# Performance work log

Measured on AMD Instinct MI355X. Metric: run time of the kernel, lower is better.

## Reference

```python
import jax, jax.numpy as jnp
import numpy as np

B, N, D = 4, 1024, 1024
H = 16
HD = D // H
FF = int(D * 2.0)
EPS = 1e-5


def setup_inputs() -> dict:
    key = jax.random.key(0)
    ks = jax.random.split(key, 12)
    s = lambda fan_in: 1.0 / np.sqrt(fan_in)
    return {
        "x": jax.random.normal(ks[0], (B, N, D), dtype=jnp.float32),
        "ln1_g": jnp.ones((D,), jnp.float32),
        "ln1_b": jnp.zeros((D,), jnp.float32),
        "qkv_w": jax.random.normal(ks[1], (D, 3 * D), jnp.float32) * s(D),
        "qkv_b": jnp.zeros((3 * D,), jnp.float32),
        "out_w": jax.random.normal(ks[2], (D, D), jnp.float32) * s(D),
        "out_b": jnp.zeros((D,), jnp.float32),
        "ln2_g": jnp.ones((D,), jnp.float32),
        "ln2_b": jnp.zeros((D,), jnp.float32),
        "w1": jax.random.normal(ks[3], (D, FF), jnp.float32) * s(D),
        "b1": jnp.zeros((FF,), jnp.float32),
        "w2": jax.random.normal(ks[4], (FF, D), jnp.float32) * s(FF),
        "b2": jnp.zeros((D,), jnp.float32),
    }


def _layernorm(x, g, b):
    mu = jnp.mean(x, axis=-1, keepdims=True)
    var = jnp.mean(jnp.square(x - mu), axis=-1, keepdims=True)
    return (x - mu) * jax.lax.rsqrt(var + EPS) * g + b


def _attention(x, qkv_w, qkv_b, out_w, out_b):
    qkv = x @ qkv_w + qkv_b                       # (B,N,3D)
    qkv = qkv.reshape(B, N, 3, H, HD)
    q, k, v = qkv[:, :, 0], qkv[:, :, 1], qkv[:, :, 2]  # (B,N,H,HD)
    scale = 1.0 / np.sqrt(HD)
    attn = jnp.einsum("bnhd,bmhd->bhnm", q, k) * scale
    attn = jax.nn.softmax(attn, axis=-1)
    out = jnp.einsum("bhnm,bmhd->bnhd", attn, v).reshape(B, N, D)
    return out @ out_w + out_b


def reference(x, ln1_g, ln1_b, qkv_w, qkv_b, out_w, out_b, ln2_g, ln2_b, w1, b1, w2, b2):
    x = x + _attention(_layernorm(x, ln1_g, ln1_b), qkv_w, qkv_b, out_w, out_b)
    h = _layernorm(x, ln2_g, ln2_b)
    h = jax.nn.gelu(h @ w1 + b1, approximate=False) @ w2 + b2
    return x + h
```

## Files before the change

kernel.cpp:

```cpp
#include <hip/hip_runtime.h>
#include <hip/hip_bf16.h>
#include <cstdint>
#include <cstddef>

#define Bq 4
#define Nseq 1024
#define Dm 1024
#define Hh 16
#define HDd 64
#define FFd 2048
#define Mrows 4096

typedef __attribute__((ext_vector_type(8))) short bf16x8;
typedef __attribute__((ext_vector_type(4))) float f32x4;
typedef __attribute__((ext_vector_type(16))) float f32x16;

__device__ __forceinline__ void gl_lds16(const void* g, void* l) {
  __builtin_amdgcn_global_load_lds(
      (const __attribute__((address_space(1))) unsigned int*)g,
      (__attribute__((address_space(3))) unsigned int*)l, 16, 0, 0);
}

__device__ __forceinline__ unsigned short f2b(float f) {
  union { __hip_bfloat16 h; unsigned short u; } cv;
  cv.h = __float2bfloat16(f);
  return cv.u;
}

__device__ __forceinline__ unsigned cvt_pk_bf16(float a, float b) {
  unsigned r;
  asm("v_cvt_pk_bf16_f32 %0, %1, %2" : "=v"(r) : "v"(a), "v"(b));
  return r;
}

__device__ __forceinline__ void pl32_swap(unsigned& a, unsigned& b) {
  asm("v_permlane32_swap_b32 %0, %1" : "+v"(a), "+v"(b));
}

__global__ __launch_bounds__(256) void transpose_cast_k(
    const float* __restrict__ src, __hip_bfloat16* __restrict__ dst,
    int K, int Ncols) {
  __shared__ float tile[32][33];
  const int n0 = blockIdx.x * 32, k0 = blockIdx.y * 32;
  const int tx = threadIdx.x & 31, ty = threadIdx.x >> 5;
#pragma unroll
  for (int i = 0; i < 32; i += 8)
    tile[ty + i][tx] = src[(size_t)(k0 + ty + i) * Ncols + n0 + tx];
  __syncthreads();
#pragma unroll
  for (int i = 0; i < 32; i += 8)
    dst[(size_t)(n0 + ty + i) * K + k0 + tx] = __float2bfloat16(tile[tx][ty + i]);
}

__global__ __launch_bounds__(256) void ln_kernel(
    const float* __restrict__ x, const float* __restrict__ gw,
    const float* __restrict__ bw, __hip_bfloat16* __restrict__ out) {
  const int row = blockIdx.x;
  const float4 v = reinterpret_cast<const float4*>(x + (size_t)row * Dm)[threadIdx.x];
  float s1 = v.x + v.y + v.z + v.w;
  float s2 = v.x * v.x + v.y * v.y + v.z * v.z + v.w * v.w;
#pragma unroll
  for (int m = 1; m < 64; m <<= 1) {
    s1 += __shfl_xor(s1, m);
    s2 += __shfl_xor(s2, m);
  }
  __shared__ float a1[4], a2[4];
  const int wv = threadIdx.x >> 6;
  if ((threadIdx.x & 63) == 0) { a1[wv] = s1; a2[wv] = s2; }
  __syncthreads();
  s1 = a1[0] + a1[1] + a1[2] + a1[3];
  s2 = a2[0] + a2[1] + a2[2] + a2[3];
  const float mu = s1 * (1.f / Dm);
  const float rs = rsqrtf(s2 * (1.f / Dm) - mu * mu + 1e-5f);
  const float4 g4 = reinterpret_cast<const float4*>(gw)[threadIdx.x];
  const float4 b4 = reinterpret_cast<const float4*>(bw)[threadIdx.x];
  ushort4 o;
  o.x = f2b((v.x - mu) * rs * g4.x + b4.x);
  o.y = f2b((v.y - mu) * rs * g4.y + b4.y);
  o.z = f2b((v.z - mu) * rs * g4.z + b4.z);
  o.w = f2b((v.w - mu) * rs * g4.w + b4.w);
  reinterpret_cast<ushort4*>(out + (size_t)row * Dm)[threadIdx.x] = o;
}

template <int EPI>
__global__ __launch_bounds__(256, 2) void gemm_bt(
    const __hip_bfloat16* __restrict__ A, const __hip_bfloat16* __restrict__ BT,
    const float* __restrict__ bias, const float* __restrict__ res,
    float* __restrict__ outF, __hip_bfloat16* __restrict__ outB,
    __hip_bfloat16* __restrict__ qb, __hip_bfloat16* __restrict__ kb,
    __hip_bfloat16* __restrict__ vtb, int Ndim, int Kdim) {
  __shared__ alignas(16) __hip_bfloat16 As[128 * 32];
  __shared__ alignas(16) __hip_bfloat16 Bs[128 * 32];
  const int tid = threadIdx.x;
  const int wv = tid >> 6, ln = tid & 63;
  const int wr = wv >> 1, wc = wv & 1;
  const int rowBase = blockIdx.y * 128;
  const int colBase = blockIdx.x * 128;

  f32x4 acc[4][4];
#pragma unroll
  for (int i = 0; i < 4; ++i)
#pragma unroll
    for (int j = 0; j < 4; ++j) acc[i][j] = {0.f, 0.f, 0.f, 0.f};

  const int lr = ln >> 2;
  const int lc = (ln & 3) * 8;
  const int fr = ln & 15, kq = (ln >> 4) * 8;

  for (int k0 = 0; k0 < Kdim; k0 += 32) {
#pragma unroll
    for (int c = 0; c < 2; ++c) {
      const int chunk = c * 4 + wv;
      gl_lds16(A + (size_t)(rowBase + chunk * 16 + lr) * Kdim + k0 + lc,
               (char*)As + chunk * 1024);
      gl_lds16(BT + (size_t)(colBase + chunk * 16 + lr) * Kdim + k0 + lc,
               (char*)Bs + chunk * 1024);
    }
    __syncthreads();
    bf16x8 af[4], bfr[4];
#pragma unroll
    for (int i = 0; i < 4; ++i)
      af[i] = *reinterpret_cast<const bf16x8*>(As + (wr * 64 + i * 16 + fr) * 32 + kq);
#pragma unroll
    for (int j = 0; j < 4; ++j)
      bfr[j] = *reinterpret_cast<const bf16x8*>(Bs + (wc * 64 + j * 16 + fr) * 32 + kq);
#pragma unroll
    for (int i = 0; i < 4; ++i)
#pragma unroll
      for (int j = 0; j < 4; ++j)
        acc[i][j] = __builtin_amdgcn_mfma_f32_16x16x32_bf16(af[i], bfr[j], acc[i][j], 0, 0, 0);
    __syncthreads();
  }

  const int rq = (ln >> 4) * 4;
#pragma unroll
  for (int i = 0; i < 4; ++i) {
#pragma unroll
    for (int j = 0; j < 4; ++j) {
      const int gc = colBase + wc * 64 + j * 16 + fr;
      const float bv = bias[gc];
#pragma unroll
      for (int ii = 0; ii < 4; ++ii) {
        const int gr = rowBase + wr * 64 + i * 16 + rq + ii;
        float v = acc[i][j][ii] + bv;
        if constexpr (EPI == 0) {
          const int which = gc >> 10;
          const int dcol = gc & 1023;
          const int h = dcol >> 6, hd = dcol & 63;
          const int b = gr >> 10, n = gr & 1023;
          const size_t bh = (size_t)(b * Hh + h);
          if (which == 0)
            qb[(bh * Nseq + n) * HDd + hd] = __float2bfloat16(v * 0.125f);
          else if (which == 1)
            kb[(bh * Nseq + n) * HDd + hd] = __float2bfloat16(v);
          else
            vtb[(bh * HDd + hd) * Nseq + n] = __float2bfloat16(v);
        } else if constexpr (EPI == 1) {
          outF[(size_t)gr * Ndim + gc] = v + res[(size_t)gr * Ndim + gc];
        } else {
          outB[(size_t)gr * Ndim + gc] =
              __float2bfloat16(0.5f * v * (1.f + erff(v * 0.70710678118f)));
        }
      }
    }
  }
}

__global__ __launch_bounds__(256, 2) void attn_kernel(
    const __hip_bfloat16* __restrict__ q, const __hip_bfloat16* __restrict__ k,
    const __hip_bfloat16* __restrict__ vt, __hip_bfloat16* __restrict__ attn) {
  __shared__ alignas(16) __hip_bfloat16 Ks[2][64 * 64];
  __shared__ alignas(16) __hip_bfloat16 Vs[2][64 * 64];
  const int tid = threadIdx.x, wv = tid >> 6, ln = tid & 63;
  const int bh = blockIdx.x >> 3, qt = blockIdx.x & 7;
  const int b = bh >> 4, h = bh & 15;
  const int lq = ln & 31;
  const int hl = ln >> 5;

  const __hip_bfloat16* kbase = k + (size_t)bh * Nseq * HDd;
  const __hip_bfloat16* vbase = vt + (size_t)bh * HDd * Nseq;

  const int st_r = ln >> 3;
  const int st_c = (ln & 7) ^ st_r;

  const __hip_bfloat16* qsrc = q + ((size_t)bh * Nseq + qt * 128 + wv * 32 + lq) * HDd;
  bf16x8 qf[4];
#pragma unroll
  for (int s = 0; s < 4; ++s)
    qf[s] = *reinterpret_cast<const bf16x8*>(qsrc + s * 16 + hl * 8);

  float mrun = -1e30f, lrun = 0.f;
  f32x16 ot0 = {}, ot1 = {};

  auto stage = [&](int buf, int kt) {
#pragma unroll
    for (int c = 0; c < 2; ++c) {
      const int chunk = wv * 2 + c;
      gl_lds16(kbase + ((size_t)kt * 64 + chunk * 8 + st_r) * HDd + st_c * 8,
               (char*)&Ks[buf][0] + chunk * 1024);
      gl_lds16(vbase + (size_t)(chunk * 8 + st_r) * Nseq + kt * 64 + st_c * 8,
               (char*)&Vs[buf][0] + chunk * 1024);
    }
  };

  stage(0, 0);
  __syncthreads();
  int cur = 0;

  for (int kt = 0; kt < 16; ++kt) {
    if (kt < 15) stage(cur ^ 1, kt + 1);

    const char* Kp = (const char*)&Ks[cur][0];
    const char* Vp = (const char*)&Vs[cur][0];

    f32x16 st0 = {}, st1 = {};
#pragma unroll
    for (int t = 0; t < 2; ++t) {
      const int row = t * 32 + lq;
#pragma unroll
      for (int s = 0; s < 4; ++s) {
        const bf16x8 kf = *reinterpret_cast<const bf16x8*>(
            Kp + row * 128 + (((s * 2 + hl) ^ (row & 7)) * 16));
        if (t == 0) st0 = __builtin_amdgcn_mfma_f32_32x32x16_bf16(kf, qf[s], st0, 0, 0, 0);
        else        st1 = __builtin_amdgcn_mfma_f32_32x32x16_bf16(kf, qf[s], st1, 0, 0, 0);
      }
    }

    float tmax = st0[0];
#pragma unroll
    for (int r = 1; r < 16; ++r) tmax = fmaxf(tmax, st0[r]);
#pragma unroll
    for (int r = 0; r < 16; ++r) tmax = fmaxf(tmax, st1[r]);
    tmax = fmaxf(tmax, __shfl_xor(tmax, 32));
    const float mn = fmaxf(mrun, tmax);
    const float sc = __expf(mrun - mn);
    mrun = mn;
    float tsum = 0.f;
#pragma unroll
    for (int r = 0; r < 16; ++r) {
      st0[r] = __expf(st0[r] - mn);
      tsum += st0[r];
    }
#pragma unroll
    for (int r = 0; r < 16; ++r) {
      st1[r] = __expf(st1[r] - mn);
      tsum += st1[r];
    }
    tsum += __shfl_xor(tsum, 32);
    lrun = lrun * sc + tsum;
#pragma unroll
    for (int r = 0; r < 16; ++r) { ot0[r] *= sc; ot1[r] *= sc; }

    union PF { unsigned u[4]; bf16x8 v; } pf[4];
#pragma unroll
    for (int t = 0; t < 2; ++t)
#pragma unroll
      for (int g = 0; g < 2; ++g) {
        unsigned w0, w1, w2, w3;
        if (t == 0) {
          w0 = cvt_pk_bf16(st0[g * 8 + 0], st0[g * 8 + 1]);
          w1 = cvt_pk_bf16(st0[g * 8 + 2], st0[g * 8 + 3]);
          w2 = cvt_pk_bf16(st0[g * 8 + 4], st0[g * 8 + 5]);
          w3 = cvt_pk_bf16(st0[g * 8 + 6], st0[g * 8 + 7]);
        } else {
          w0 = cvt_pk_bf16(st1[g * 8 + 0], st1[g * 8 + 1]);
          w1 = cvt_pk_bf16(st1[g * 8 + 2], st1[g * 8 + 3]);
          w2 = cvt_pk_bf16(st1[g * 8 + 4], st1[g * 8 + 5]);
          w3 = cvt_pk_bf16(st1[g * 8 + 6], st1[g * 8 + 7]);
        }
        pl32_swap(w0, w2);
        pl32_swap(w1, w3);
        PF f;
        f.u[0] = w0; f.u[1] = w1; f.u[2] = w2; f.u[3] = w3;
        pf[t * 2 + g] = f;
      }

#pragma unroll
    for (int dt = 0; dt < 2; ++dt) {
      const int row = dt * 32 + lq;
#pragma unroll
      for (int ks = 0; ks < 4; ++ks) {
        const bf16x8 vf = *reinterpret_cast<const bf16x8*>(
            Vp + row * 128 + (((ks * 2 + hl) ^ (row & 7)) * 16));
        if (dt == 0) ot0 = __builtin_amdgcn_mfma_f32_32x32x16_bf16(vf, pf[ks].v, ot0, 0, 0, 0);
        else         ot1 = __builtin_amdgcn_mfma_f32_32x32x16_bf16(vf, pf[ks].v, ot1, 0, 0, 0);
      }
    }

    __syncthreads();
    cur ^= 1;
  }

  const float inv = 1.f / lrun;
  char* swb = (char*)(&Ks[0][0] + wv * 2048);
#pragma unroll
  for (int dt = 0; dt < 2; ++dt)
#pragma unroll
    for (int i = 0; i < 8; ++i) {
      const unsigned w = (dt == 0)
          ? cvt_pk_bf16(ot0[2 * i] * inv, ot0[2 * i + 1] * inv)
          : cvt_pk_bf16(ot1[2 * i] * inv, ot1[2 * i + 1] * inv);
      const int d0 = (2 * i & 2) + 8 * (i >> 1) + 4 * hl + 32 * dt;
      *(unsigned*)(swb + lq * 128 + (((d0 >> 3) ^ (lq & 7)) * 16) + (d0 & 7) * 2) = w;
    }
  const int brow = b * Nseq + qt * 128 + wv * 32;
#pragma unroll
  for (int it = 0; it < 4; ++it) {
    const int qr = it * 8 + (ln >> 3);
    const bf16x8 o = *reinterpret_cast<const bf16x8*>(
        swb + qr * 128 + (((ln & 7) ^ (qr & 7)) * 16));
    *reinterpret_cast<bf16x8*>(attn + (size_t)(brow + qr) * Dm + h * 64 + (ln & 7) * 8) = o;
  }
}

extern "C" void kernel_launch(void* const* d_in, const int* in_sizes, int n_in,
                              void* d_out, int out_size, void* d_ws, size_t ws_size,
                              hipStream_t stream) {
  (void)in_sizes; (void)n_in; (void)out_size; (void)ws_size;
  const float* x     = (const float*)d_in[0];
  const float* ln1_g = (const float*)d_in[1];
  const float* ln1_b = (const float*)d_in[2];
  const float* qkv_w = (const float*)d_in[3];
  const float* qkv_b = (const float*)d_in[4];
  const float* out_w = (const float*)d_in[5];
  const float* out_b = (const float*)d_in[6];
  const float* ln2_g = (const float*)d_in[7];
  const float* ln2_b = (const float*)d_in[8];
  const float* w1    = (const float*)d_in[9];
  const float* b1    = (const float*)d_in[10];
  const float* w2    = (const float*)d_in[11];
  const float* b2    = (const float*)d_in[12];
  float* outp = (float*)d_out;

  char* ws = (char*)d_ws;
  size_t off = 0;
  auto take = [&](size_t bytes) {
    char* p = ws + off;
    off += (bytes + 255) & ~(size_t)255;
    return p;
  };
  __hip_bfloat16* wqkv_t = (__hip_bfloat16*)take((size_t)3 * Dm * Dm * 2);
  __hip_bfloat16* wout_t = (__hip_bfloat16*)take((size_t)Dm * Dm * 2);
  __hip_bfloat16* w1_t   = (__hip_bfloat16*)take((size_t)FFd * Dm * 2);
  __hip_bfloat16* w2_t   = (__hip_bfloat16*)take((size_t)Dm * FFd * 2);
  __hip_bfloat16* xn     = (__hip_bfloat16*)take((size_t)Mrows * Dm * 2);
  __hip_bfloat16* qb     = (__hip_bfloat16*)take((size_t)Mrows * Dm * 2);
  __hip_bfloat16* kb     = (__hip_bfloat16*)take((size_t)Mrows * Dm * 2);
  __hip_bfloat16* vtb    = (__hip_bfloat16*)take((size_t)Mrows * Dm * 2);
  __hip_bfloat16* attn   = (__hip_bfloat16*)take((size_t)Mrows * Dm * 2);
  float*          x1     = (float*)take((size_t)Mrows * Dm * 4);
  __hip_bfloat16* gbuf   = (__hip_bfloat16*)take((size_t)Mrows * FFd * 2);

  const dim3 blk(256);
  transpose_cast_k<<<dim3(3 * Dm / 32, Dm / 32), blk, 0, stream>>>(qkv_w, wqkv_t, Dm, 3 * Dm);
  transpose_cast_k<<<dim3(Dm / 32, Dm / 32), blk, 0, stream>>>(out_w, wout_t, Dm, Dm);
  transpose_cast_k<<<dim3(FFd / 32, Dm / 32), blk, 0, stream>>>(w1, w1_t, Dm, FFd);
  transpose_cast_k<<<dim3(Dm / 32, FFd / 32), blk, 0, stream>>>(w2, w2_t, FFd, Dm);
  ln_kernel<<<dim3(Mrows), blk, 0, stream>>>(x, ln1_g, ln1_b, xn);
  gemm_bt<0><<<dim3(3 * Dm / 128, Mrows / 128), blk, 0, stream>>>(
      xn, wqkv_t, qkv_b, nullptr, nullptr, nullptr, qb, kb, vtb, 3 * Dm, Dm);
  attn_kernel<<<dim3(Bq * Hh * (Nseq / 128)), blk, 0, stream>>>(qb, kb, vtb, attn);
  gemm_bt<1><<<dim3(Dm / 128, Mrows / 128), blk, 0, stream>>>(
      attn, wout_t, out_b, x, x1, nullptr, nullptr, nullptr, nullptr, Dm, Dm);
  ln_kernel<<<dim3(Mrows), blk, 0, stream>>>(x1, ln2_g, ln2_b, xn);
  gemm_bt<2><<<dim3(FFd / 128, Mrows / 128), blk, 0, stream>>>(
      xn, w1_t, b1, nullptr, nullptr, gbuf, nullptr, nullptr, nullptr, FFd, Dm);
  gemm_bt<1><<<dim3(Dm / 128, Mrows / 128), blk, 0, stream>>>(
      gbuf, w2_t, b2, x1, outp, nullptr, nullptr, nullptr, nullptr, Dm, FFd);
}
```

Baseline: 202.4 us.

## Double-buffer GEMM LDS tiles with swizzle and 32x32x16 MFMA

Reworks the bf16 GEMM main loop. It widens the K tile from 32 to 64, double-buffers the A/B tiles in LDS so the next tile's global-to-LDS load overlaps the current MFMAs, and XOR-swizzles the LDS layout to avoid bank conflicts. It also switches from 16x16x32 to 32x32x16 MFMA with a matching epilogue row mapping. LDS use per block grows fourfold, which with launch bounds of 2 blocks per CU may limit occupancy, and the single barrier per iteration relies on async load ordering for correctness.

```diff
diff --git a/kernel.cpp b/kernel.cpp
--- a/kernel.cpp
+++ b/kernel.cpp
@@ -89,60 +89,79 @@
     float* __restrict__ outF, __hip_bfloat16* __restrict__ outB,
     __hip_bfloat16* __restrict__ qb, __hip_bfloat16* __restrict__ kb,
     __hip_bfloat16* __restrict__ vtb, int Ndim, int Kdim) {
-  __shared__ alignas(16) __hip_bfloat16 As[128 * 32];
-  __shared__ alignas(16) __hip_bfloat16 Bs[128 * 32];
+  __shared__ alignas(16) __hip_bfloat16 As[2][128 * 64];
+  __shared__ alignas(16) __hip_bfloat16 Bs[2][128 * 64];
   const int tid = threadIdx.x;
   const int wv = tid >> 6, ln = tid & 63;
   const int wr = wv >> 1, wc = wv & 1;
+  const int lq = ln & 31, hl = ln >> 5;
   const int rowBase = blockIdx.y * 128;
   const int colBase = blockIdx.x * 128;
 
-  f32x4 acc[4][4];
-#pragma unroll
-  for (int i = 0; i < 4; ++i)
-#pragma unroll
-    for (int j = 0; j < 4; ++j) acc[i][j] = {0.f, 0.f, 0.f, 0.f};
-
-  const int lr = ln >> 2;
-  const int lc = (ln & 3) * 8;
-  const int fr = ln & 15, kq = (ln >> 4) * 8;
-
-  for (int k0 = 0; k0 < Kdim; k0 += 32) {
-#pragma unroll
-    for (int c = 0; c < 2; ++c) {
-      const int chunk = c * 4 + wv;
-      gl_lds16(A + (size_t)(rowBase + chunk * 16 + lr) * Kdim + k0 + lc,
-               (char*)As + chunk * 1024);
-      gl_lds16(BT + (size_t)(colBase + chunk * 16 + lr) * Kdim + k0 + lc,
-               (char*)Bs + chunk * 1024);
+  const int st_r = ln >> 3;
+  const int st_c = (ln & 7) ^ st_r;
+
+  f32x16 acc[2][2];
+#pragma unroll
+  for (int i = 0; i < 2; ++i)
+#pragma unroll
+    for (int j = 0; j < 2; ++j) acc[i][j] = {};
+
+  auto stage = [&](int buf, int k0) {
+#pragma unroll
+    for (int c = 0; c < 4; ++c) {
+      const int grp = wv * 4 + c;
+      gl_lds16(A + (size_t)(rowBase + grp * 8 + st_r) * Kdim + k0 + st_c * 8,
+               (char*)&As[buf][0] + grp * 1024);
+      gl_lds16(BT + (size_t)(colBase + grp * 8 + st_r) * Kdim + k0 + st_c * 8,
+               (char*)&Bs[buf][0] + grp * 1024);
+    }
+  };
+
+  stage(0, 0);
+  __syncthreads();
+  int cur = 0;
+  const int nt = Kdim >> 6;
+
+  for (int kt = 0; kt < nt; ++kt) {
+    if (kt + 1 < nt) stage(cur ^ 1, (kt + 1) << 6);
+    const char* Ap = (const char*)&As[cur][0];
+    const char* Bp = (const char*)&Bs[cur][0];
+#pragma unroll
+    for (int ks = 0; ks < 4; ++ks) {
+      bf16x8 af[2], bfr[2];
+#pragma unroll
+      for (int i = 0; i < 2; ++i) {
+        const int row = wr * 64 + i * 32 + lq;
+        af[i] = *reinterpret_cast<const bf16x8*>(
+            Ap + row * 128 + (((ks * 2 + hl) ^ (lq & 7)) * 16));
+      }
+#pragma unroll
+      for (int j = 0; j < 2; ++j) {
+        const int row = wc * 64 + j * 32 + lq;
+        bfr[j] = *reinterpret_cast<const bf16x8*>(
+            Bp + row * 128 + (((ks * 2 + hl) ^ (lq & 7)) * 16));
+      }
+#pragma unroll
+      for (int i = 0; i < 2; ++i)
+#pragma unroll
+        for (int j = 0; j < 2; ++j)
+          acc[i][j] = __builtin_amdgcn_mfma_f32_32x32x16_bf16(af[i], bfr[j], acc[i][j], 0, 0, 0);
     }
     __syncthreads();
-    bf16x8 af[4], bfr[4];
-#pragma unroll
-    for (int i = 0; i < 4; ++i)
-      af[i] = *reinterpret_cast<const bf16x8*>(As + (wr * 64 + i * 16 + fr) * 32 + kq);
-#pragma unroll
-    for (int j = 0; j < 4; ++j)
-      bfr[j] = *reinterpret_cast<const bf16x8*>(Bs + (wc * 64 + j * 16 + fr) * 32 + kq);
-#pragma unroll
-    for (int i = 0; i < 4; ++i)
-#pragma unroll
-      for (int j = 0; j < 4; ++j)
-        acc[i][j] = __builtin_amdgcn_mfma_f32_16x16x32_bf16(af[i], bfr[j], acc[i][j], 0, 0, 0);
-    __syncthreads();
-  }
-
-  const int rq = (ln >> 4) * 4;
-#pragma unroll
-  for (int i = 0; i < 4; ++i) {
-#pragma unroll
-    for (int j = 0; j < 4; ++j) {
-      const int gc = colBase + wc * 64 + j * 16 + fr;
+    cur ^= 1;
+  }
+
+#pragma unroll
+  for (int i = 0; i < 2; ++i) {
+#pragma unroll
+    for (int j = 0; j < 2; ++j) {
+      const int gc = colBase + wc * 64 + j * 32 + lq;
       const float bv = bias[gc];
 #pragma unroll
-      for (int ii = 0; ii < 4; ++ii) {
-        const int gr = rowBase + wr * 64 + i * 16 + rq + ii;
-        float v = acc[i][j][ii] + bv;
+      for (int r = 0; r < 16; ++r) {
+        const int gr = rowBase + wr * 64 + i * 32 + (r & 3) + 8 * (r >> 2) + 4 * hl;
+        float v = acc[i][j][r] + bv;
         if constexpr (EPI == 0) {
           const int which = gc >> 10;
           const int dcol = gc & 1023;
```

After: 206.3 us. Within noise of the previous version (+1.9%).

## Add 256x128 triple-buffered 32x32 MFMA GEMM for QKV and FFN1

Applied to the files above, without the earlier changes.

Adds a new 512-thread GEMM kernel with 256x128 tiles, BK=64, a three-stage global-to-LDS prefetch pipeline, XOR-swizzled LDS layout and 32x32x16 MFMA. It is used for the QKV projection and the first FFN matmul. The goal is better data reuse, hidden load latency and fewer LDS bank conflicts on the two largest GEMMs. The trade-off is much higher LDS use (about 144 KB per block), only one block per CU, and fewer blocks overall, which may hurt occupancy and tail balance.

```diff
diff --git a/kernel.cpp b/kernel.cpp
--- a/kernel.cpp
+++ b/kernel.cpp
@@ -87,8 +87,7 @@
     const __hip_bfloat16* __restrict__ A, const __hip_bfloat16* __restrict__ BT,
     const float* __restrict__ bias, const float* __restrict__ res,
     float* __restrict__ outF, __hip_bfloat16* __restrict__ outB,
-    __hip_bfloat16* __restrict__ qb, __hip_bfloat16* __restrict__ kb,
-    __hip_bfloat16* __restrict__ vtb, int Ndim, int Kdim) {
+    int Ndim, int Kdim) {
   __shared__ alignas(16) __hip_bfloat16 As[128 * 32];
   __shared__ alignas(16) __hip_bfloat16 Bs[128 * 32];
   const int tid = threadIdx.x;
@@ -143,6 +142,112 @@
       for (int ii = 0; ii < 4; ++ii) {
         const int gr = rowBase + wr * 64 + i * 16 + rq + ii;
         float v = acc[i][j][ii] + bv;
+        if constexpr (EPI == 1) {
+          outF[(size_t)gr * Ndim + gc] = v + res[(size_t)gr * Ndim + gc];
+        } else {
+          outB[(size_t)gr * Ndim + gc] =
+              __float2bfloat16(0.5f * v * (1.f + erff(v * 0.70710678118f)));
+        }
+      }
+    }
+  }
+}
+
+template <int EPI>
+__global__ __launch_bounds__(512, 1) void gemm8(
+    const __hip_bfloat16* __restrict__ A, const __hip_bfloat16* __restrict__ BT,
+    const float* __restrict__ bias,
+    __hip_bfloat16* __restrict__ outB,
+    __hip_bfloat16* __restrict__ qb, __hip_bfloat16* __restrict__ kb,
+    __hip_bfloat16* __restrict__ vtb, int Ndim, int Kdim) {
+  __shared__ alignas(16) __hip_bfloat16 As[3][256 * 64];
+  __shared__ alignas(16) __hip_bfloat16 Bs[3][128 * 64];
+  const int tid = threadIdx.x;
+  const int ln = tid & 63;
+  const int w = tid >> 6;
+  const int wm = w >> 1, wn = w & 1;
+  const int lq = ln & 31, hl = ln >> 5;
+  const int rowBase = blockIdx.y * 256;
+  const int colBase = blockIdx.x * 128;
+  const int st_row = tid >> 3;
+  const int st_c = (tid & 7) ^ (st_row & 7);
+  const int nt = Kdim >> 6;
+
+  f32x16 acc[2][2];
+#pragma unroll
+  for (int i = 0; i < 2; ++i)
+#pragma unroll
+    for (int j = 0; j < 2; ++j) acc[i][j] = {};
+
+  auto stageA = [&](int slot, int kt2, int r) {
+    gl_lds16(A + (size_t)(rowBase + r * 64 + st_row) * Kdim + (kt2 << 6) + st_c * 8,
+             (char*)&As[slot][0] + r * 8192 + tid * 16);
+  };
+  auto stageB = [&](int slot, int kt2, int r) {
+    gl_lds16(BT + (size_t)(colBase + r * 64 + st_row) * Kdim + (kt2 << 6) + st_c * 8,
+             (char*)&Bs[slot][0] + r * 8192 + tid * 16);
+  };
+
+#pragma unroll
+  for (int r = 0; r < 4; ++r) stageA(0, 0, r);
+#pragma unroll
+  for (int r = 0; r < 2; ++r) stageB(0, 0, r);
+#pragma unroll
+  for (int r = 0; r < 4; ++r) stageA(1, 1, r);
+#pragma unroll
+  for (int r = 0; r < 2; ++r) stageB(1, 1, r);
+  asm volatile("s_waitcnt vmcnt(6)" ::: "memory");
+  __builtin_amdgcn_s_barrier();
+
+  for (int kt = 0; kt < nt; ++kt) {
+    const int slot = kt % 3;
+    const int nslot = (kt + 2) % 3;
+    const bool pf = (kt + 2) < nt;
+    const char* Ap = (const char*)&As[slot][0];
+    const char* Bp = (const char*)&Bs[slot][0];
+#pragma unroll
+    for (int ks = 0; ks < 4; ++ks) {
+      if (ks == 0 && pf) { stageA(nslot, kt + 2, 0); stageA(nslot, kt + 2, 1); }
+      if (ks == 1 && pf) { stageA(nslot, kt + 2, 2); stageA(nslot, kt + 2, 3); }
+      if (ks == 2 && pf) { stageB(nslot, kt + 2, 0); stageB(nslot, kt + 2, 1); }
+      bf16x8 af[2], bfr[2];
+#pragma unroll
+      for (int i = 0; i < 2; ++i)
+        af[i] = *reinterpret_cast<const bf16x8*>(
+            Ap + (wm * 64 + i * 32 + lq) * 128 + (((ks * 2 + hl) ^ (lq & 7)) * 16));
+#pragma unroll
+      for (int j = 0; j < 2; ++j)
+        bfr[j] = *reinterpret_cast<const bf16x8*>(
+            Bp + (wn * 64 + j * 32 + lq) * 128 + (((ks * 2 + hl) ^ (lq & 7)) * 16));
+      __builtin_amdgcn_s_barrier();
+      __builtin_amdgcn_s_setprio(1);
+#pragma unroll
+      for (int i = 0; i < 2; ++i)
+#pragma unroll
+        for (int j = 0; j < 2; ++j)
+          acc[i][j] = __builtin_amdgcn_mfma_f32_32x32x16_bf16(af[i], bfr[j], acc[i][j], 0, 0, 0);
+      __builtin_amdgcn_s_setprio(0);
+      if (ks == 3) {
+        if (pf) {
+          asm volatile("s_waitcnt vmcnt(6)" ::: "memory");
+        } else if (kt + 1 < nt) {
+          asm volatile("s_waitcnt vmcnt(0)" ::: "memory");
+        }
+      }
+      __builtin_amdgcn_s_barrier();
+    }
+  }
+
+#pragma unroll
+  for (int i = 0; i < 2; ++i) {
+#pragma unroll
+    for (int j = 0; j < 2; ++j) {
+      const int gc = colBase + wn * 64 + j * 32 + lq;
+      const float bv = bias[gc];
+#pragma unroll
+      for (int r = 0; r < 16; ++r) {
+        const int gr = rowBase + wm * 64 + i * 32 + (r & 3) + 8 * (r >> 2) + 4 * hl;
+        float v = acc[i][j][r] + bv;
         if constexpr (EPI == 0) {
           const int which = gc >> 10;
           const int dcol = gc & 1023;
@@ -155,8 +260,6 @@
             kb[(bh * Nseq + n) * HDd + hd] = __float2bfloat16(v);
           else
             vtb[(bh * HDd + hd) * Nseq + n] = __float2bfloat16(v);
-        } else if constexpr (EPI == 1) {
-          outF[(size_t)gr * Ndim + gc] = v + res[(size_t)gr * Ndim + gc];
         } else {
           outB[(size_t)gr * Ndim + gc] =
               __float2bfloat16(0.5f * v * (1.f + erff(v * 0.70710678118f)));
@@ -357,14 +460,14 @@
   transpose_cast_k<<<dim3(FFd / 32, Dm / 32), blk, 0, stream>>>(w1, w1_t, Dm, FFd);
   transpose_cast_k<<<dim3(Dm / 32, FFd / 32), blk, 0, stream>>>(w2, w2_t, FFd, Dm);
   ln_kernel<<<dim3(Mrows), blk, 0, stream>>>(x, ln1_g, ln1_b, xn);
-  gemm_bt<0><<<dim3(3 * Dm / 128, Mrows / 128), blk, 0, stream>>>(
-      xn, wqkv_t, qkv_b, nullptr, nullptr, nullptr, qb, kb, vtb, 3 * Dm, Dm);
+  gemm8<0><<<dim3(3 * Dm / 128, Mrows / 256), dim3(512), 0, stream>>>(
+      xn, wqkv_t, qkv_b, nullptr, qb, kb, vtb, 3 * Dm, Dm);
   attn_kernel<<<dim3(Bq * Hh * (Nseq / 128)), blk, 0, stream>>>(qb, kb, vtb, attn);
   gemm_bt<1><<<dim3(Dm / 128, Mrows / 128), blk, 0, stream>>>(
-      attn, wout_t, out_b, x, x1, nullptr, nullptr, nullptr, nullptr, Dm, Dm);
+      attn, wout_t, out_b, x, x1, nullptr, Dm, Dm);
   ln_kernel<<<dim3(Mrows), blk, 0, stream>>>(x1, ln2_g, ln2_b, xn);
-  gemm_bt<2><<<dim3(FFd / 128, Mrows / 128), blk, 0, stream>>>(
-      xn, w1_t, b1, nullptr, nullptr, gbuf, nullptr, nullptr, nullptr, FFd, Dm);
+  gemm8<2><<<dim3(FFd / 128, Mrows / 256), dim3(512), 0, stream>>>(
+      xn, w1_t, b1, gbuf, nullptr, nullptr, nullptr, FFd, Dm);
   gemm_bt<1><<<dim3(Dm / 128, Mrows / 128), blk, 0, stream>>>(
-      gbuf, w2_t, b2, x1, outp, nullptr, nullptr, nullptr, nullptr, Dm, FFd);
-}
+      gbuf, w2_t, b2, x1, outp, nullptr, Dm, FFd);
+}
```

After: 257.0 us. 27.0% more time.
